# Kernel optimization log

Measured on AMD Instinct MI355X. Metric: run time of the kernel, lower is better.

Reference implementation:

```python
import jax, jax.numpy as jnp
import numpy as np

B, S, D, H = 8, 1024, 768, 12
DH = D // H


def setup_inputs() -> dict:
    key = jax.random.key(0)
    ks = jax.random.split(key, 6)
    scale = 1.0 / np.sqrt(D)
    return {
        "inputs": jax.random.normal(ks[0], (B, S, D), dtype=jnp.float32),
        "Wq": jax.random.normal(ks[1], (D, D), dtype=jnp.float32) * scale,
        "bq": jnp.zeros((D,), jnp.float32),
        "Wk": jax.random.normal(ks[2], (D, D), dtype=jnp.float32) * scale,
        "bk": jnp.zeros((D,), jnp.float32),
        "Wv": jax.random.normal(ks[3], (D, D), dtype=jnp.float32) * scale,
        "bv": jnp.zeros((D,), jnp.float32),
        "Wo": jax.random.normal(ks[4], (D, D), dtype=jnp.float32) * scale,
        "bo": jnp.zeros((D,), jnp.float32),
    }


def _split_heads(x):
    # [B,S,D] -> [B,H,S,DH]
    b, s, _ = x.shape
    return x.reshape(b, s, H, DH).transpose(0, 2, 1, 3)


def reference(inputs, Wq, bq, Wk, bk, Wv, bv, Wo, bo):
    q = _split_heads(inputs @ Wq + bq)
    k = _split_heads(inputs @ Wk + bk)
    v = _split_heads(inputs @ Wv + bv)
    # scaled dot-product attention; scale = sqrt(projection_dim)
    scores = jnp.einsum("bhqd,bhkd->bhqk", q, k) / jnp.sqrt(jnp.float32(DH))
    weights = jax.nn.softmax(scores, axis=-1)
    attn = jnp.einsum("bhqk,bhkd->bhqd", weights, v)
    attn = attn.transpose(0, 2, 1, 3).reshape(inputs.shape[0], -1, D)
    return attn @ Wo + bo
```

## Files before the change

### kernel.cpp

```cpp
#include <hip/hip_runtime.h>
#include <math.h>

#define B 8
#define S 1024
#define D 768
#define H 12
#define DH 64
#define M_TOT (B * S)

typedef short bf16x8 __attribute__((ext_vector_type(8)));
typedef float f32x4 __attribute__((ext_vector_type(4)));

__device__ __forceinline__ unsigned short f2bf(float x) {
    unsigned u = __builtin_bit_cast(unsigned, x);
    u = (u + 0x7FFFu + ((u >> 16) & 1u)) >> 16;
    return (unsigned short)u;
}
__device__ __forceinline__ unsigned pk2bf(float a, float b) {
    return (unsigned)f2bf(a) | ((unsigned)f2bf(b) << 16);
}

__device__ __forceinline__ void async16(const unsigned short* g, unsigned short* l) {
    __builtin_amdgcn_global_load_lds((const __attribute__((address_space(1))) void*)g,
                                     (__attribute__((address_space(3))) void*)l, 16, 0, 0);
}

__global__ __launch_bounds__(256) void conv_bf16(const float* __restrict__ src,
                                                 unsigned short* __restrict__ dst) {
    const int i = (blockIdx.x * 256 + threadIdx.x) * 4;
    const float4 v = *(const float4*)&src[i];
    ushort4 o;
    o.x = f2bf(v.x); o.y = f2bf(v.y); o.z = f2bf(v.z); o.w = f2bf(v.w);
    *(ushort4*)&dst[i] = o;
}

__global__ __launch_bounds__(256) void wtrans(const float* W0, const float* W1,
                                              const float* W2, const float* W3,
                                              unsigned short* T0, unsigned short* T1,
                                              unsigned short* T2, unsigned short* T3) {
    const float* Wsrc[4] = {W0, W1, W2, W3};
    unsigned short* Tdst[4] = {T0, T1, T2, T3};
    const float* Wm = Wsrc[blockIdx.z];
    unsigned short* Tm = Tdst[blockIdx.z];
    __shared__ float tile[64][65];
    const int t = threadIdx.x;
    const int r = t >> 4, c4 = (t & 15) * 4;
    const int k0 = blockIdx.x * 64, n0 = blockIdx.y * 64;
#pragma unroll
    for (int rr = 0; rr < 4; ++rr) {
        const float4 v = *(const float4*)&Wm[(size_t)(k0 + r + rr * 16) * D + n0 + c4];
        tile[r + rr * 16][c4 + 0] = v.x;
        tile[r + rr * 16][c4 + 1] = v.y;
        tile[r + rr * 16][c4 + 2] = v.z;
        tile[r + rr * 16][c4 + 3] = v.w;
    }
    __syncthreads();
#pragma unroll
    for (int rr = 0; rr < 4; ++rr) {
        const int nr = r + rr * 16;
        ushort4 o;
        o.x = f2bf(tile[c4 + 0][nr]);
        o.y = f2bf(tile[c4 + 1][nr]);
        o.z = f2bf(tile[c4 + 2][nr]);
        o.w = f2bf(tile[c4 + 3][nr]);
        *(ushort4*)&Tm[(size_t)(n0 + nr) * D + k0 + c4] = o;
    }
}

__global__ __launch_bounds__(256) void gemm_qkv(const unsigned short* __restrict__ A,
                                                const unsigned short* __restrict__ Wtq,
                                                const unsigned short* __restrict__ Wtk,
                                                const unsigned short* __restrict__ Wtv,
                                                const float* __restrict__ bq,
                                                const float* __restrict__ bk,
                                                const float* __restrict__ bv,
                                                unsigned short* __restrict__ Qb,
                                                unsigned short* __restrict__ Kb,
                                                unsigned short* __restrict__ Vtb) {
    __shared__ unsigned short At[128 * 32];
    __shared__ unsigned short Bs[128 * 32];
    const int z = blockIdx.z;
    const unsigned short* Bt = (z == 0) ? Wtq : (z == 1) ? Wtk : Wtv;
    const float* bias = (z == 0) ? bq : (z == 1) ? bk : bv;
    const float scale = (z == 0) ? 0.125f : 1.0f;

    const int t = threadIdx.x;
    const int w = t >> 6, lane = t & 63;
    const int quad = lane >> 4, l15 = lane & 15;
    const int m0 = blockIdx.x * 128, n0 = blockIdx.y * 128;
    const int wm = (w & 1) * 64, wn = (w >> 1) * 64;
    const int srow = lane >> 2, scol = (lane & 3) * 8;

    f32x4 acc[4][4];
#pragma unroll
    for (int i = 0; i < 4; ++i)
#pragma unroll
        for (int j = 0; j < 4; ++j) acc[i][j] = (f32x4){0.f, 0.f, 0.f, 0.f};

    for (int kt = 0; kt < D / 32; ++kt) {
        const int k0 = kt * 32;
        __syncthreads();
#pragma unroll
        for (int c = 0; c < 2; ++c) {
            const int cc = w * 2 + c;
            const int row = cc * 16 + srow;
            async16(&A[(size_t)(m0 + row) * D + k0 + scol], &At[cc * 512]);
            async16(&Bt[(size_t)(n0 + row) * D + k0 + scol], &Bs[cc * 512]);
        }
        __syncthreads();
        bf16x8 af[4], bfr[4];
#pragma unroll
        for (int i = 0; i < 4; ++i)
            af[i] = *(const bf16x8*)&At[(wm + i * 16 + l15) * 32 + quad * 8];
#pragma unroll
        for (int j = 0; j < 4; ++j)
            bfr[j] = *(const bf16x8*)&Bs[(wn + j * 16 + l15) * 32 + quad * 8];
#pragma unroll
        for (int i = 0; i < 4; ++i)
#pragma unroll
            for (int j = 0; j < 4; ++j)
                acc[i][j] = __builtin_amdgcn_mfma_f32_16x16x32_bf16(af[i], bfr[j], acc[i][j], 0, 0, 0);
    }

#pragma unroll
    for (int j = 0; j < 4; ++j) {
        const int col = n0 + wn + j * 16 + l15;
        const float bv2 = bias[col];
#pragma unroll
        for (int i = 0; i < 4; ++i) {
            const int row0 = m0 + wm + i * 16 + quad * 4;
            if (z < 2) {
                unsigned short* C = (z == 0) ? Qb : Kb;
#pragma unroll
                for (int r = 0; r < 4; ++r)
                    C[(size_t)(row0 + r) * D + col] = f2bf((acc[i][j][r] + bv2) * scale);
            } else {
                const int h = col >> 6, dh = col & 63;
                const int bb = row0 >> 10, s0 = row0 & 1023;
                ushort4 o;
                o.x = f2bf(acc[i][j][0] + bv2);
                o.y = f2bf(acc[i][j][1] + bv2);
                o.z = f2bf(acc[i][j][2] + bv2);
                o.w = f2bf(acc[i][j][3] + bv2);
                *(ushort4*)&Vtb[((size_t)(bb * H + h) * DH + dh) * S + s0] = o;
            }
        }
    }
}

__global__ __launch_bounds__(256) void gemm_out(const unsigned short* __restrict__ A,
                                                const unsigned short* __restrict__ Bt,
                                                const float* __restrict__ bias,
                                                float* __restrict__ C) {
    __shared__ unsigned short At[128 * 32];
    __shared__ unsigned short Bs[128 * 32];
    const int t = threadIdx.x;
    const int w = t >> 6, lane = t & 63;
    const int quad = lane >> 4, l15 = lane & 15;
    const int m0 = blockIdx.x * 128, n0 = blockIdx.y * 128;
    const int wm = (w & 1) * 64, wn = (w >> 1) * 64;
    const int srow = lane >> 2, scol = (lane & 3) * 8;

    f32x4 acc[4][4];
#pragma unroll
    for (int i = 0; i < 4; ++i)
#pragma unroll
        for (int j = 0; j < 4; ++j) acc[i][j] = (f32x4){0.f, 0.f, 0.f, 0.f};

    for (int kt = 0; kt < D / 32; ++kt) {
        const int k0 = kt * 32;
        __syncthreads();
#pragma unroll
        for (int c = 0; c < 2; ++c) {
            const int cc = w * 2 + c;
            const int row = cc * 16 + srow;
            async16(&A[(size_t)(m0 + row) * D + k0 + scol], &At[cc * 512]);
            async16(&Bt[(size_t)(n0 + row) * D + k0 + scol], &Bs[cc * 512]);
        }
        __syncthreads();
        bf16x8 af[4], bfr[4];
#pragma unroll
        for (int i = 0; i < 4; ++i)
            af[i] = *(const bf16x8*)&At[(wm + i * 16 + l15) * 32 + quad * 8];
#pragma unroll
        for (int j = 0; j < 4; ++j)
            bfr[j] = *(const bf16x8*)&Bs[(wn + j * 16 + l15) * 32 + quad * 8];
#pragma unroll
        for (int i = 0; i < 4; ++i)
#pragma unroll
            for (int j = 0; j < 4; ++j)
                acc[i][j] = __builtin_amdgcn_mfma_f32_16x16x32_bf16(af[i], bfr[j], acc[i][j], 0, 0, 0);
    }

#pragma unroll
    for (int j = 0; j < 4; ++j) {
        const int col = n0 + wn + j * 16 + l15;
        const float bv = bias[col];
#pragma unroll
        for (int i = 0; i < 4; ++i) {
            const int row0 = m0 + wm + i * 16 + quad * 4;
#pragma unroll
            for (int r = 0; r < 4; ++r) C[(size_t)(row0 + r) * D + col] = acc[i][j][r] + bv;
        }
    }
}

__global__ __launch_bounds__(256) void attn_mfma(const unsigned short* __restrict__ Qg,
                                                 const unsigned short* __restrict__ Kg,
                                                 const unsigned short* __restrict__ Vtg,
                                                 unsigned short* __restrict__ ATT) {
    __shared__ unsigned short Ks[2 * 64 * 32];
    __shared__ unsigned short Vs[2 * 64 * 32];
    __shared__ unsigned short Ps2[4 * 16 * 72];

    const int t = threadIdx.x;
    const int w = t >> 6, lane = t & 63;
    const int quad = lane >> 4, l15 = lane & 15;
    const int bh = blockIdx.x % (B * H);
    const int q0 = (blockIdx.x / (B * H)) * 64;
    const int b = bh / H, h = bh % H;

    const size_t qoff = ((size_t)(b * S + q0 + w * 16 + l15)) * D + h * DH;
    const bf16x8 qa0 = *(const bf16x8*)&Qg[qoff + quad * 8];
    const bf16x8 qa1 = *(const bf16x8*)&Qg[qoff + 32 + quad * 8];

    f32x4 o[4];
#pragma unroll
    for (int n = 0; n < 4; ++n) o[n] = (f32x4){0.f, 0.f, 0.f, 0.f};
    float m_r = -INFINITY, l_r = 0.f;

    const int srow = lane >> 2, scol = (lane & 3) * 8;
    unsigned short* myP = &Ps2[w * 16 * 72];

    for (int kt = 0; kt < S / 64; ++kt) {
        __syncthreads();
#pragma unroll
        for (int kc = 0; kc < 2; ++kc) {
            async16(&Kg[((size_t)(b * S + kt * 64 + w * 16 + srow)) * D + h * DH + kc * 32 + scol],
                    &Ks[kc * 2048 + w * 512]);
            async16(&Vtg[((size_t)(bh * DH + w * 16 + srow)) * S + kt * 64 + kc * 32 + scol],
                    &Vs[kc * 2048 + w * 512]);
        }
        __syncthreads();

        f32x4 sc[4];
#pragma unroll
        for (int n = 0; n < 4; ++n) {
            const bf16x8 ka0 = *(const bf16x8*)&Ks[0 * 2048 + (n * 16 + l15) * 32 + quad * 8];
            const bf16x8 ka1 = *(const bf16x8*)&Ks[1 * 2048 + (n * 16 + l15) * 32 + quad * 8];
            f32x4 zz = (f32x4){0.f, 0.f, 0.f, 0.f};
            zz = __builtin_amdgcn_mfma_f32_16x16x32_bf16(ka0, qa0, zz, 0, 0, 0);
            zz = __builtin_amdgcn_mfma_f32_16x16x32_bf16(ka1, qa1, zz, 0, 0, 0);
            sc[n] = zz;
        }

        float rmax = -INFINITY;
#pragma unroll
        for (int n = 0; n < 4; ++n)
#pragma unroll
            for (int r = 0; r < 4; ++r) rmax = fmaxf(rmax, sc[n][r]);
        rmax = fmaxf(rmax, __shfl_xor(rmax, 16, 64));
        rmax = fmaxf(rmax, __shfl_xor(rmax, 32, 64));
        const float mnew = fmaxf(m_r, rmax);
        const float alpha = __expf(m_r - mnew);
        m_r = mnew;
        float p[4][4];
        float rsum = 0.f;
#pragma unroll
        for (int n = 0; n < 4; ++n)
#pragma unroll
            for (int r = 0; r < 4; ++r) {
                p[n][r] = __expf(sc[n][r] - mnew);
                rsum += p[n][r];
            }
        rsum += __shfl_xor(rsum, 16, 64);
        rsum += __shfl_xor(rsum, 32, 64);
        l_r = l_r * alpha + rsum;

#pragma unroll
        for (int n = 0; n < 4; ++n) o[n] *= alpha;

#pragma unroll
        for (int n = 0; n < 4; ++n) {
            uint2 u;
            u.x = pk2bf(p[n][0], p[n][1]);
            u.y = pk2bf(p[n][2], p[n][3]);
            *(uint2*)&myP[l15 * 72 + n * 16 + quad * 4] = u;
        }
        __asm__ volatile("s_waitcnt lgkmcnt(0)" ::: "memory");

        const bf16x8 pb0 = *(const bf16x8*)&myP[l15 * 72 + 0 + quad * 8];
        const bf16x8 pb1 = *(const bf16x8*)&myP[l15 * 72 + 32 + quad * 8];

#pragma unroll
        for (int n = 0; n < 4; ++n) {
            const bf16x8 va0 = *(const bf16x8*)&Vs[0 * 2048 + (n * 16 + l15) * 32 + quad * 8];
            const bf16x8 va1 = *(const bf16x8*)&Vs[1 * 2048 + (n * 16 + l15) * 32 + quad * 8];
            o[n] = __builtin_amdgcn_mfma_f32_16x16x32_bf16(va0, pb0, o[n], 0, 0, 0);
            o[n] = __builtin_amdgcn_mfma_f32_16x16x32_bf16(va1, pb1, o[n], 0, 0, 0);
        }
    }

    const float inv = 1.0f / l_r;
    const size_t row = (size_t)(b * S + q0 + w * 16 + l15) * D + h * DH;
#pragma unroll
    for (int n = 0; n < 4; ++n) {
        ushort4 ov;
        ov.x = f2bf(o[n][0] * inv);
        ov.y = f2bf(o[n][1] * inv);
        ov.z = f2bf(o[n][2] * inv);
        ov.w = f2bf(o[n][3] * inv);
        *(ushort4*)&ATT[row + n * 16 + quad * 4] = ov;
    }
}

extern "C" void kernel_launch(void* const* d_in, const int* in_sizes, int n_in,
                              void* d_out, int out_size, void* d_ws, size_t ws_size,
                              hipStream_t stream) {
    const float* inputs = (const float*)d_in[0];
    const float* Wq = (const float*)d_in[1];
    const float* bq = (const float*)d_in[2];
    const float* Wk = (const float*)d_in[3];
    const float* bk = (const float*)d_in[4];
    const float* Wv = (const float*)d_in[5];
    const float* bv = (const float*)d_in[6];
    const float* Wo = (const float*)d_in[7];
    const float* bo = (const float*)d_in[8];

    const size_t nA = (size_t)M_TOT * D;
    unsigned short* Abf  = (unsigned short*)d_ws;
    unsigned short* Qb   = Abf + nA;
    unsigned short* Kb   = Qb + nA;
    unsigned short* Vtb  = Kb + nA;
    unsigned short* ATTb = Vtb + nA;
    unsigned short* Wtq  = ATTb + nA;
    unsigned short* Wtk  = Wtq + (size_t)D * D;
    unsigned short* Wtv  = Wtk + (size_t)D * D;
    unsigned short* Wto  = Wtv + (size_t)D * D;

    conv_bf16<<<M_TOT * D / 1024, 256, 0, stream>>>(inputs, Abf);
    wtrans<<<dim3(D / 64, D / 64, 4), 256, 0, stream>>>(Wq, Wk, Wv, Wo, Wtq, Wtk, Wtv, Wto);

    gemm_qkv<<<dim3(M_TOT / 128, D / 128, 3), 256, 0, stream>>>(
        Abf, Wtq, Wtk, Wtv, bq, bk, bv, Qb, Kb, Vtb);

    attn_mfma<<<dim3((S / 64) * B * H), 256, 0, stream>>>(Qb, Kb, Vtb, ATTb);

    gemm_out<<<dim3(M_TOT / 128, D / 128), 256, 0, stream>>>(ATTb, Wto, bo, (float*)d_out);
}
```

Measured before the change: 239.6 us.

## Process two query tiles per wave in attention and swizzle K/V LDS layout

Each wave now computes 32 query rows instead of 16, so every K and V fragment read from LDS feeds two MFMA chains and each block covers 128 queries. This halves K/V global-to-LDS traffic per query and halves the grid size. An XOR swizzle is applied to the K/V LDS placement and reads to reduce bank conflicts. It raises register pressure and reduces the number of blocks available to fill the GPU.

```diff
diff --git a/kernel.cpp b/kernel.cpp
--- a/kernel.cpp
+++ b/kernel.cpp
@@ -211,26 +211,36 @@
                                                  unsigned short* __restrict__ ATT) {
     __shared__ unsigned short Ks[2 * 64 * 32];
     __shared__ unsigned short Vs[2 * 64 * 32];
-    __shared__ unsigned short Ps2[4 * 16 * 72];
+    __shared__ unsigned short Ps2[4 * 32 * 72];
 
     const int t = threadIdx.x;
     const int w = t >> 6, lane = t & 63;
     const int quad = lane >> 4, l15 = lane & 15;
     const int bh = blockIdx.x % (B * H);
-    const int q0 = (blockIdx.x / (B * H)) * 64;
+    const int q0 = (blockIdx.x / (B * H)) * 128;
     const int b = bh / H, h = bh % H;
 
-    const size_t qoff = ((size_t)(b * S + q0 + w * 16 + l15)) * D + h * DH;
-    const bf16x8 qa0 = *(const bf16x8*)&Qg[qoff + quad * 8];
-    const bf16x8 qa1 = *(const bf16x8*)&Qg[qoff + 32 + quad * 8];
-
-    f32x4 o[4];
-#pragma unroll
-    for (int n = 0; n < 4; ++n) o[n] = (f32x4){0.f, 0.f, 0.f, 0.f};
-    float m_r = -INFINITY, l_r = 0.f;
-
-    const int srow = lane >> 2, scol = (lane & 3) * 8;
-    unsigned short* myP = &Ps2[w * 16 * 72];
+    bf16x8 qb[2][2];
+#pragma unroll
+    for (int qh = 0; qh < 2; ++qh) {
+        const size_t qoff = ((size_t)(b * S + q0 + w * 32 + qh * 16 + l15)) * D + h * DH;
+        qb[qh][0] = *(const bf16x8*)&Qg[qoff + quad * 8];
+        qb[qh][1] = *(const bf16x8*)&Qg[qoff + 32 + quad * 8];
+    }
+
+    f32x4 o[2][4];
+#pragma unroll
+    for (int qh = 0; qh < 2; ++qh)
+#pragma unroll
+        for (int n = 0; n < 4; ++n) o[qh][n] = (f32x4){0.f, 0.f, 0.f, 0.f};
+    float m_r[2] = {-INFINITY, -INFINITY};
+    float l_r[2] = {0.f, 0.f};
+
+    const int srow = lane >> 2;
+    const int scol = (((lane & 3) ^ ((lane >> 3) & 3))) * 8;
+    const int fsw = ((quad ^ ((l15 >> 1) & 3)) * 8);
+
+    unsigned short* myP = &Ps2[w * 32 * 72];
 
     for (int kt = 0; kt < S / 64; ++kt) {
         __syncthreads();
@@ -243,74 +253,86 @@
         }
         __syncthreads();
 
-        f32x4 sc[4];
+        f32x4 sc[2][4];
 #pragma unroll
         for (int n = 0; n < 4; ++n) {
-            const bf16x8 ka0 = *(const bf16x8*)&Ks[0 * 2048 + (n * 16 + l15) * 32 + quad * 8];
-            const bf16x8 ka1 = *(const bf16x8*)&Ks[1 * 2048 + (n * 16 + l15) * 32 + quad * 8];
-            f32x4 zz = (f32x4){0.f, 0.f, 0.f, 0.f};
-            zz = __builtin_amdgcn_mfma_f32_16x16x32_bf16(ka0, qa0, zz, 0, 0, 0);
-            zz = __builtin_amdgcn_mfma_f32_16x16x32_bf16(ka1, qa1, zz, 0, 0, 0);
-            sc[n] = zz;
-        }
-
-        float rmax = -INFINITY;
-#pragma unroll
-        for (int n = 0; n < 4; ++n)
-#pragma unroll
-            for (int r = 0; r < 4; ++r) rmax = fmaxf(rmax, sc[n][r]);
-        rmax = fmaxf(rmax, __shfl_xor(rmax, 16, 64));
-        rmax = fmaxf(rmax, __shfl_xor(rmax, 32, 64));
-        const float mnew = fmaxf(m_r, rmax);
-        const float alpha = __expf(m_r - mnew);
-        m_r = mnew;
-        float p[4][4];
-        float rsum = 0.f;
-#pragma unroll
-        for (int n = 0; n < 4; ++n)
-#pragma unroll
-            for (int r = 0; r < 4; ++r) {
-                p[n][r] = __expf(sc[n][r] - mnew);
-                rsum += p[n][r];
+            const bf16x8 ka0 = *(const bf16x8*)&Ks[0 * 2048 + (n * 16 + l15) * 32 + fsw];
+            const bf16x8 ka1 = *(const bf16x8*)&Ks[1 * 2048 + (n * 16 + l15) * 32 + fsw];
+#pragma unroll
+            for (int qh = 0; qh < 2; ++qh) {
+                f32x4 zz = (f32x4){0.f, 0.f, 0.f, 0.f};
+                zz = __builtin_amdgcn_mfma_f32_16x16x32_bf16(ka0, qb[qh][0], zz, 0, 0, 0);
+                zz = __builtin_amdgcn_mfma_f32_16x16x32_bf16(ka1, qb[qh][1], zz, 0, 0, 0);
+                sc[qh][n] = zz;
             }
-        rsum += __shfl_xor(rsum, 16, 64);
-        rsum += __shfl_xor(rsum, 32, 64);
-        l_r = l_r * alpha + rsum;
-
-#pragma unroll
-        for (int n = 0; n < 4; ++n) o[n] *= alpha;
+        }
+
+        float alpha[2];
+#pragma unroll
+        for (int qh = 0; qh < 2; ++qh) {
+            float rmax = -INFINITY;
+#pragma unroll
+            for (int n = 0; n < 4; ++n)
+#pragma unroll
+                for (int r = 0; r < 4; ++r) rmax = fmaxf(rmax, sc[qh][n][r]);
+            rmax = fmaxf(rmax, __shfl_xor(rmax, 16, 64));
+            rmax = fmaxf(rmax, __shfl_xor(rmax, 32, 64));
+            const float mnew = fmaxf(m_r[qh], rmax);
+            alpha[qh] = __expf(m_r[qh] - mnew);
+            m_r[qh] = mnew;
+            float rsum = 0.f;
+#pragma unroll
+            for (int n = 0; n < 4; ++n) {
+                uint2 u;
+                float p0 = __expf(sc[qh][n][0] - mnew);
+                float p1 = __expf(sc[qh][n][1] - mnew);
+                float p2 = __expf(sc[qh][n][2] - mnew);
+                float p3 = __expf(sc[qh][n][3] - mnew);
+                rsum += (p0 + p1) + (p2 + p3);
+                u.x = pk2bf(p0, p1);
+                u.y = pk2bf(p2, p3);
+                *(uint2*)&myP[(qh * 16 + l15) * 72 + n * 16 + quad * 4] = u;
+            }
+            rsum += __shfl_xor(rsum, 16, 64);
+            rsum += __shfl_xor(rsum, 32, 64);
+            l_r[qh] = l_r[qh] * alpha[qh] + rsum;
+#pragma unroll
+            for (int n = 0; n < 4; ++n) o[qh][n] *= alpha[qh];
+        }
+        __asm__ volatile("s_waitcnt lgkmcnt(0)" ::: "memory");
+
+        bf16x8 pb[2][2];
+#pragma unroll
+        for (int qh = 0; qh < 2; ++qh) {
+            pb[qh][0] = *(const bf16x8*)&myP[(qh * 16 + l15) * 72 + 0 + quad * 8];
+            pb[qh][1] = *(const bf16x8*)&myP[(qh * 16 + l15) * 72 + 32 + quad * 8];
+        }
 
 #pragma unroll
         for (int n = 0; n < 4; ++n) {
-            uint2 u;
-            u.x = pk2bf(p[n][0], p[n][1]);
-            u.y = pk2bf(p[n][2], p[n][3]);
-            *(uint2*)&myP[l15 * 72 + n * 16 + quad * 4] = u;
-        }
-        __asm__ volatile("s_waitcnt lgkmcnt(0)" ::: "memory");
-
-        const bf16x8 pb0 = *(const bf16x8*)&myP[l15 * 72 + 0 + quad * 8];
-        const bf16x8 pb1 = *(const bf16x8*)&myP[l15 * 72 + 32 + quad * 8];
-
+            const bf16x8 va0 = *(const bf16x8*)&Vs[0 * 2048 + (n * 16 + l15) * 32 + fsw];
+            const bf16x8 va1 = *(const bf16x8*)&Vs[1 * 2048 + (n * 16 + l15) * 32 + fsw];
+#pragma unroll
+            for (int qh = 0; qh < 2; ++qh) {
+                o[qh][n] = __builtin_amdgcn_mfma_f32_16x16x32_bf16(va0, pb[qh][0], o[qh][n], 0, 0, 0);
+                o[qh][n] = __builtin_amdgcn_mfma_f32_16x16x32_bf16(va1, pb[qh][1], o[qh][n], 0, 0, 0);
+            }
+        }
+    }
+
+#pragma unroll
+    for (int qh = 0; qh < 2; ++qh) {
+        const float inv = 1.0f / l_r[qh];
+        const size_t row = (size_t)(b * S + q0 + w * 32 + qh * 16 + l15) * D + h * DH;
 #pragma unroll
         for (int n = 0; n < 4; ++n) {
-            const bf16x8 va0 = *(const bf16x8*)&Vs[0 * 2048 + (n * 16 + l15) * 32 + quad * 8];
-            const bf16x8 va1 = *(const bf16x8*)&Vs[1 * 2048 + (n * 16 + l15) * 32 + quad * 8];
-            o[n] = __builtin_amdgcn_mfma_f32_16x16x32_bf16(va0, pb0, o[n], 0, 0, 0);
-            o[n] = __builtin_amdgcn_mfma_f32_16x16x32_bf16(va1, pb1, o[n], 0, 0, 0);
-        }
-    }
-
-    const float inv = 1.0f / l_r;
-    const size_t row = (size_t)(b * S + q0 + w * 16 + l15) * D + h * DH;
-#pragma unroll
-    for (int n = 0; n < 4; ++n) {
-        ushort4 ov;
-        ov.x = f2bf(o[n][0] * inv);
-        ov.y = f2bf(o[n][1] * inv);
-        ov.z = f2bf(o[n][2] * inv);
-        ov.w = f2bf(o[n][3] * inv);
-        *(ushort4*)&ATT[row + n * 16 + quad * 4] = ov;
+            ushort4 ov;
+            ov.x = f2bf(o[qh][n][0] * inv);
+            ov.y = f2bf(o[qh][n][1] * inv);
+            ov.z = f2bf(o[qh][n][2] * inv);
+            ov.w = f2bf(o[qh][n][3] * inv);
+            *(ushort4*)&ATT[row + n * 16 + quad * 4] = ov;
+        }
     }
 }
 
@@ -344,7 +366,7 @@
     gemm_qkv<<<dim3(M_TOT / 128, D / 128, 3), 256, 0, stream>>>(
         Abf, Wtq, Wtk, Wtv, bq, bk, bv, Qb, Kb, Vtb);
 
-    attn_mfma<<<dim3((S / 64) * B * H), 256, 0, stream>>>(Qb, Kb, Vtb, ATTb);
+    attn_mfma<<<dim3((S / 128) * B * H), 256, 0, stream>>>(Qb, Kb, Vtb, ATTb);
 
     gemm_out<<<dim3(M_TOT / 128, D / 128), 256, 0, stream>>>(ATTb, Wto, bo, (float*)d_out);
 }
```

Result: faster. 231.6 us (-3.3%).
